# Kernel tuning notes

Hardware: AMD Instinct MI355X
Metric: run time of the kernel (lower is better)

Reference implementation:

```python
import jax, jax.numpy as jnp
import numpy as np
jax.config.update("jax_enable_x64", True)

N_ITER = 5
B, N = 64, 128

_C1 = jnp.uint64(0x9E3779B97F4A7C15)
_C2 = jnp.uint64(0xBF58476D1CE4E5B9)
_C3 = jnp.uint64(0x94D049BB133111EB)
_SALT = jnp.uint64(0xD1B54A32D192ED03)


def _mix(x):
    # splitmix64 finalizer: a bijection on uint64 -> preserves label equality classes
    z = x + _C1
    z = (z ^ (z >> jnp.uint64(30))) * _C2
    z = (z ^ (z >> jnp.uint64(27))) * _C3
    return z ^ (z >> jnp.uint64(31))


def setup_inputs() -> dict:
    key = jax.random.key(0)
    k1, k2 = jax.random.split(key)
    u = jax.random.uniform(k1, (B, N, N))
    adj = jnp.where(u < 0.06, 1.0, 0.0).astype(jnp.float32)
    adj = jnp.maximum(adj, jnp.transpose(adj, (0, 2, 1)))  # symmetric
    eye = jnp.eye(N, dtype=jnp.float32)
    adj = adj * (1.0 - eye)  # no self loops
    labels = jax.random.randint(k2, (B, N), 0, 10, dtype=jnp.int32)
    return {"adj": adj, "labels": labels}


def _kernel_contrib(h):
    # h: [B, N] uint64 labels. K[i,j] = #{(u,v): label_u == label_v}
    L = h.reshape(-1)                                   # [T]
    eq = (L[:, None] == L[None, :]).astype(jnp.float32)  # [T, T]
    return eq.reshape(B, N, B, N).sum(axis=(1, 3))       # [B, B]


def reference(adj, labels):
    adj_u = (adj > 0.5).astype(jnp.uint64)        # [B, N, N]
    h = _mix(labels.astype(jnp.uint64))           # initial labels (bijective relabel)
    K = _kernel_contrib(h)
    for _ in range(N_ITER):
        # commutative multiset hash of neighbor labels
        nsum = jnp.einsum('bij,bj->bi', adj_u, _mix(h ^ _SALT))
        # combine own label with neighbor multiset -> WL relabel
        h = _mix(_mix(h) + nsum)
        K = K + _kernel_contrib(h)
    d = jnp.sqrt(jnp.diag(K))
    return K / (d[:, None] * d[None, :])
```

## Files before the change

### kernel.cpp

```cpp
#include <hip/hip_runtime.h>

typedef unsigned long long u64;
typedef unsigned int u32;

#define NB 64
#define NN 128
#define NITER 5
#define NGEN 6
#define SALT 0xD1B54A32D192ED03ULL
#define NPAIR_OFF (NB*(NB-1)/2)
#define TSLOTS 256

__device__ __forceinline__ u64 mix64(u64 x) {
    u64 z = x + 0x9E3779B97F4A7C15ULL;
    z = (z ^ (z >> 30)) * 0xBF58476D1CE4E5B9ULL;
    z = (z ^ (z >> 27)) * 0x94D049BB133111EBULL;
    return z ^ (z >> 31);
}

__global__ __launch_bounds__(512) void wl_iter(const float* __restrict__ adj,
                                               const int* __restrict__ labels,
                                               u32* __restrict__ hgen32,
                                               float* __restrict__ out) {
    const int b = blockIdx.x;
    const int t = threadIdx.x;
    const int u = t & 127;
    const int q = t >> 7;

    __shared__ u64 gsh[NN];
    __shared__ u64 psum[3][NN];

    const float* rowp = adj + ((size_t)b * NN + u) * NN + q * 32;
    u32 m = 0;
    #pragma unroll
    for (int k = 0; k < 8; ++k) {
        const float4 v = *(const float4*)(rowp + 4 * k);
        m |= (v.x > 0.5f ? 1u : 0u) << (4 * k);
        m |= (v.y > 0.5f ? 1u : 0u) << (4 * k + 1);
        m |= (v.z > 0.5f ? 1u : 0u) << (4 * k + 2);
        m |= (v.w > 0.5f ? 1u : 0u) << (4 * k + 3);
    }

    u64 h = 0;
    if (q == 0) {
        h = mix64((u64)(u32)labels[b * NN + u]);
        hgen32[(size_t)b * (NGEN * NN) + u] = (u32)h;
        if (u == 0) out[b * NB + b] = 1.0f;
    }

    for (int it = 0; it < NITER; ++it) {
        if (q == 0) gsh[u] = mix64(h ^ SALT);
        __syncthreads();
        u64 s = 0;
        {
            u32 mm = m;
            const u64* gp = gsh + q * 32;
            while (mm) { int j = __builtin_ctz(mm); mm &= mm - 1; s += gp[j]; }
        }
        if (q) psum[q - 1][u] = s;
        __syncthreads();
        if (q == 0) {
            h = mix64(mix64(h) + s + psum[0][u] + psum[1][u] + psum[2][u]);
            hgen32[(size_t)b * (NGEN * NN) + (it + 1) * NN + u] = (u32)h;
        }
    }
}

__global__ __launch_bounds__(128) void wl_tables(const u32* __restrict__ hgen32,
                                                 uint2* __restrict__ tabg,
                                                 float* __restrict__ Kpart) {
    const int bg = blockIdx.x;
    const int t = threadIdx.x;

    __shared__ u32 keys[TSLOTS];
    __shared__ u32 cnts[TSLOTS];
    keys[t] = 0u; keys[t + 128] = 0u;
    cnts[t] = 0u; cnts[t + 128] = 0u;
    __syncthreads();

    const u32 h = hgen32[(size_t)bg * NN + t];
    u32 s = h & (TSLOTS - 1);
    for (;;) {
        u32 old = atomicCAS(&keys[s], 0u, h);
        if (old == 0u || old == h) { atomicAdd(&cnts[s], 1u); break; }
        s = (s + 1) & (TSLOTS - 1);
    }
    __syncthreads();

    u32 acc = 0;
    #pragma unroll
    for (int k = 0; k < 2; ++k) {
        const int idx = t + 128 * k;
        const u32 kk = keys[idx];
        const u32 cc = cnts[idx];
        tabg[(size_t)bg * TSLOTS + idx] = make_uint2(kk, cc);
        acc += cc * cc;
    }
    #pragma unroll
    for (int off = 32; off > 0; off >>= 1) acc += __shfl_down(acc, off);
    __shared__ u32 part[2];
    if ((t & 63) == 0) part[t >> 6] = acc;
    __syncthreads();
    if (t == 0) Kpart[bg] = (float)(part[0] + part[1]);
}

__global__ __launch_bounds__(256) void wl_pairs(const u32* __restrict__ hgen32,
                                                const uint2* __restrict__ tabg,
                                                const float* __restrict__ Kpart,
                                                float* __restrict__ out) {
    const int p = blockIdx.x;
    int b1 = (int)((1.0f + sqrtf(1.0f + 8.0f * (float)p)) * 0.5f);
    while (b1 * (b1 - 1) / 2 > p) --b1;
    while ((b1 + 1) * b1 / 2 <= p) ++b1;
    const int b2 = p - b1 * (b1 - 1) / 2;

    const int t = threadIdx.x;
    __shared__ uint2 tab[NGEN * TSLOTS];
    __shared__ u32 red[4];
    __shared__ float dred[2 * NGEN];

    if (t < 2 * NGEN)
        dred[t] = Kpart[(t < NGEN ? b1 : b2) * NGEN + (t % NGEN)];

    {
        const uint4* src = (const uint4*)(tabg + (size_t)b2 * NGEN * TSLOTS);
        uint4* dst = (uint4*)tab;
        #pragma unroll
        for (int k = 0; k < 3; ++k) dst[t + 256 * k] = src[t + 256 * k];
    }
    __syncthreads();

    u32 c = 0;
    const u32* la = hgen32 + (size_t)b1 * (NGEN * NN);
    #pragma unroll
    for (int k = 0; k < 3; ++k) {
        const int idx = t + 256 * k;
        const u32 a = la[idx];
        const int base = (idx >> 7) * TSLOTS;
        u32 s = a & (TSLOTS - 1);
        for (;;) {
            const uint2 kv = tab[base + s];
            if (kv.x == a) { c += kv.y; break; }
            if (kv.x == 0u) break;
            s = (s + 1) & (TSLOTS - 1);
        }
    }

    #pragma unroll
    for (int off = 32; off > 0; off >>= 1) c += __shfl_down(c, off);
    if ((t & 63) == 0) red[t >> 6] = c;
    __syncthreads();
    if (t == 0) {
        float d1 = 0.f, d2 = 0.f;
        #pragma unroll
        for (int g = 0; g < NGEN; ++g) { d1 += dred[g]; d2 += dred[NGEN + g]; }
        const float v = (float)(red[0] + red[1] + red[2] + red[3])
                      / (sqrtf(d1) * sqrtf(d2));
        out[b1 * NB + b2] = v;
        out[b2 * NB + b1] = v;
    }
}

extern "C" void kernel_launch(void* const* d_in, const int* in_sizes, int n_in,
                              void* d_out, int out_size, void* d_ws, size_t ws_size,
                              hipStream_t stream) {
    const float* adj   = (const float*)d_in[0];
    const int*  labels = (const int*)d_in[1];
    float* out = (float*)d_out;

    char* ws = (char*)d_ws;
    u32*   hgen32 = (u32*)ws;
    uint2* tabg   = (uint2*)(ws + 256 * 1024);
    float* Kpart  = (float*)(ws + 1536 * 1024);

    wl_iter  <<<NB, 512, 0, stream>>>(adj, labels, hgen32, out);
    wl_tables<<<NB * NGEN, 128, 0, stream>>>(hgen32, tabg, Kpart);
    wl_pairs <<<NPAIR_OFF, 256, 0, stream>>>(hgen32, tabg, Kpart, out);
}
```

Measured before the change: 26.83 us.

## Reduce neighbor sums via lane shuffles and probe hash tables from global memory

In the WL iteration kernel, threads are remapped so the four quarter-row workers for each node sit in adjacent lanes. Their partial neighbor sums are combined with xor shuffles instead of a shared-memory array and a second barrier per iteration, and a double-buffered label array removes the remaining hazard. All four lanes now compute the label redundantly. In the pairs kernel, the per-block copy of the 12 KB hash table into shared memory and its barrier are dropped, and probes read the table directly from global memory, relying on L2/L1 caching.

```diff
diff --git a/kernel.cpp b/kernel.cpp
--- a/kernel.cpp
+++ b/kernel.cpp
@@ -24,13 +24,13 @@
                                                float* __restrict__ out) {
     const int b = blockIdx.x;
     const int t = threadIdx.x;
-    const int u = t & 127;
-    const int q = t >> 7;
+    const int l = t & 63;
+    const int n = ((t >> 6) << 4) + (l >> 2);
+    const int q = l & 3;
 
-    __shared__ u64 gsh[NN];
-    __shared__ u64 psum[3][NN];
+    __shared__ u64 gsh[2][NN];
 
-    const float* rowp = adj + ((size_t)b * NN + u) * NN + q * 32;
+    const float* rowp = adj + ((size_t)b * NN + n) * NN + q * 32;
     u32 m = 0;
     #pragma unroll
     for (int k = 0; k < 8; ++k) {
@@ -41,28 +41,25 @@
         m |= (v.w > 0.5f ? 1u : 0u) << (4 * k + 3);
     }
 
-    u64 h = 0;
+    u64 h = mix64((u64)(u32)labels[b * NN + n]);
     if (q == 0) {
-        h = mix64((u64)(u32)labels[b * NN + u]);
-        hgen32[(size_t)b * (NGEN * NN) + u] = (u32)h;
-        if (u == 0) out[b * NB + b] = 1.0f;
+        hgen32[(size_t)b * (NGEN * NN) + n] = (u32)h;
+        if (n == 0) out[b * NB + b] = 1.0f;
     }
 
     for (int it = 0; it < NITER; ++it) {
-        if (q == 0) gsh[u] = mix64(h ^ SALT);
+        if (q == 0) gsh[it & 1][n] = mix64(h ^ SALT);
         __syncthreads();
         u64 s = 0;
         {
             u32 mm = m;
-            const u64* gp = gsh + q * 32;
+            const u64* gp = gsh[it & 1] + q * 32;
             while (mm) { int j = __builtin_ctz(mm); mm &= mm - 1; s += gp[j]; }
         }
-        if (q) psum[q - 1][u] = s;
-        __syncthreads();
-        if (q == 0) {
-            h = mix64(mix64(h) + s + psum[0][u] + psum[1][u] + psum[2][u]);
-            hgen32[(size_t)b * (NGEN * NN) + (it + 1) * NN + u] = (u32)h;
-        }
+        s += (u64)__shfl_xor((long long)s, 1);
+        s += (u64)__shfl_xor((long long)s, 2);
+        h = mix64(mix64(h) + s);
+        if (q == 0) hgen32[(size_t)b * (NGEN * NN) + (it + 1) * NN + n] = (u32)h;
     }
 }
 
@@ -115,23 +112,15 @@
     const int b2 = p - b1 * (b1 - 1) / 2;
 
     const int t = threadIdx.x;
-    __shared__ uint2 tab[NGEN * TSLOTS];
     __shared__ u32 red[4];
     __shared__ float dred[2 * NGEN];
 
     if (t < 2 * NGEN)
         dred[t] = Kpart[(t < NGEN ? b1 : b2) * NGEN + (t % NGEN)];
 
-    {
-        const uint4* src = (const uint4*)(tabg + (size_t)b2 * NGEN * TSLOTS);
-        uint4* dst = (uint4*)tab;
-        #pragma unroll
-        for (int k = 0; k < 3; ++k) dst[t + 256 * k] = src[t + 256 * k];
-    }
-    __syncthreads();
-
     u32 c = 0;
     const u32* la = hgen32 + (size_t)b1 * (NGEN * NN);
+    const uint2* tb = tabg + (size_t)b2 * (NGEN * TSLOTS);
     #pragma unroll
     for (int k = 0; k < 3; ++k) {
         const int idx = t + 256 * k;
@@ -139,7 +128,7 @@
         const int base = (idx >> 7) * TSLOTS;
         u32 s = a & (TSLOTS - 1);
         for (;;) {
-            const uint2 kv = tab[base + s];
+            const uint2 kv = tb[base + s];
             if (kv.x == a) { c += kv.y; break; }
             if (kv.x == 0u) break;
             s = (s + 1) & (TSLOTS - 1);
```

Measured after the change: 29.45 us. 9.8% more time.
